# Kernel tuning notes

Hardware: AMD Instinct MI355X
Metric: run time of the kernel (lower is better)

The kernel has to match this reference:

```python
import jax, jax.numpy as jnp
import numpy as np
import math

NUM_HEAD = 16
HEAD_DIM = 64  # hidden_dim 1024 / 16 heads


def setup_inputs() -> dict:
    key = jax.random.key(0)
    ks = jax.random.split(key, 7)
    N, D = 4096, 1024
    s = 1.0 / math.sqrt(D)
    return {
        "node_emb": jax.random.normal(ks[0], (N, D), jnp.float32),
        "Wq": jax.random.normal(ks[1], (D, D), jnp.float32) * s,
        "bq": jax.random.normal(ks[2], (D,), jnp.float32) * 0.01,
        "Wk": jax.random.normal(ks[3], (D, D), jnp.float32) * s,
        "bk": jax.random.normal(ks[4], (D,), jnp.float32) * 0.01,
        "Wv": jax.random.normal(ks[5], (D, D), jnp.float32) * s,
        "bv": jax.random.normal(ks[6], (D,), jnp.float32) * 0.01,
    }


def reference(node_emb, Wq, bq, Wk, bk, Wv, bv):
    N = node_emb.shape[0]
    # QKV projections (Linear: x @ W^T-style; here W stored [in, out])
    q = (node_emb @ Wq + bq).reshape(N, NUM_HEAD, HEAD_DIM)
    k = (node_emb @ Wk + bk).reshape(N, NUM_HEAD, HEAD_DIM)
    v = (node_emb @ Wv + bv).reshape(N, NUM_HEAD, HEAD_DIM)
    # scores: [h, n_query, n_key]
    scale = 1.0 / math.sqrt(HEAD_DIM)
    scores = jnp.einsum("nhd,mhd->hnm", q, k) * scale
    attn = jax.nn.softmax(scores, axis=-1)
    out = jnp.einsum("hnm,mhd->nhd", attn, v)  # [n, h, d]
    return out.reshape(N, NUM_HEAD * HEAD_DIM)
```

## Files before the change

### kernel.cpp

```cpp
#include <hip/hip_runtime.h>
#include <hip/hip_bf16.h>

#define N_NODES 4096
#define DMODEL  1024
#define NHEAD   16
#define HDIM    64
#define NOUT    3072

typedef __attribute__((ext_vector_type(8))) short short8v;
typedef __attribute__((ext_vector_type(4))) float f32x4;
typedef __attribute__((ext_vector_type(16))) float f32x16;
typedef __attribute__((ext_vector_type(4))) unsigned short ushort4v;
typedef __attribute__((ext_vector_type(4))) unsigned int u32x4;

static __device__ __forceinline__ void gload_lds16(const void* g, void* l) {
  __builtin_amdgcn_global_load_lds((const __attribute__((address_space(1))) void*)g,
                                   (__attribute__((address_space(3))) void*)l, 16, 0, 0);
}

static __device__ __forceinline__ unsigned cvtpk(float a, float b) {
  unsigned r;
  asm("v_cvt_pk_bf16_f32 %0, %1, %2" : "=v"(r) : "v"(a), "v"(b));
  return r;
}

__global__ void cvt_x_kernel(const float* __restrict__ x, __hip_bfloat16* __restrict__ xb) {
  int i = blockIdx.x * blockDim.x + threadIdx.x;
  float4 v = ((const float4*)x)[i];
  union { ushort4v u; __hip_bfloat16 h[4]; } o;
  o.h[0] = __float2bfloat16(v.x);
  o.h[1] = __float2bfloat16(v.y);
  o.h[2] = __float2bfloat16(v.z);
  o.h[3] = __float2bfloat16(v.w);
  ((ushort4v*)xb)[i] = o.u;
}

__global__ void transpose_w_kernel(const float* __restrict__ Wq, const float* __restrict__ Wk,
                                   const float* __restrict__ Wv, __hip_bfloat16* __restrict__ WT) {
  __shared__ float tile[32][33];
  const float* W = blockIdx.z == 0 ? Wq : (blockIdx.z == 1 ? Wk : Wv);
  int o0 = blockIdx.x * 32, i0 = blockIdx.y * 32;
  int tx = threadIdx.x, ty = threadIdx.y;
#pragma unroll
  for (int j = 0; j < 32; j += 8)
    tile[ty + j][tx] = W[(size_t)(i0 + ty + j) * DMODEL + o0 + tx];
  __syncthreads();
  __hip_bfloat16* outp = WT + (size_t)blockIdx.z * DMODEL * DMODEL;
#pragma unroll
  for (int j = 0; j < 32; j += 8)
    outp[(size_t)(o0 + ty + j) * DMODEL + i0 + tx] = __float2bfloat16(tile[tx][ty + j]);
}

__global__ __launch_bounds__(256, 2) void gemm_qkv_kernel(
    const __hip_bfloat16* __restrict__ X, const __hip_bfloat16* __restrict__ WT,
    const float* __restrict__ bq, const float* __restrict__ bk, const float* __restrict__ bv,
    __hip_bfloat16* __restrict__ Qo, __hip_bfloat16* __restrict__ Ko, __hip_bfloat16* __restrict__ Vt) {
  __shared__ __hip_bfloat16 As[128 * 32];
  __shared__ __hip_bfloat16 Bs[128 * 32];
  const int t = threadIdx.x;
  const int lane = t & 63;
  const int w = t >> 6, wr = w >> 1, wc = w & 1;
  const int bm = blockIdx.y, bn = blockIdx.x;

  f32x4 acc[4][4] = {};

  const int rowA = t >> 2;
  const int koff = (t & 3) * 8;
  const __hip_bfloat16* Ag0 = X + (size_t)(bm * 128 + rowA) * DMODEL + koff;
  const __hip_bfloat16* Ag1 = X + (size_t)(bm * 128 + 64 + rowA) * DMODEL + koff;
  const __hip_bfloat16* Bg0 = WT + (size_t)(bn * 128 + rowA) * DMODEL + koff;
  const __hip_bfloat16* Bg1 = WT + (size_t)(bn * 128 + 64 + rowA) * DMODEL + koff;
  __hip_bfloat16* Al0 = &As[t * 8];
  __hip_bfloat16* Al1 = &As[(t + 256) * 8];
  __hip_bfloat16* Bl0 = &Bs[t * 8];
  __hip_bfloat16* Bl1 = &Bs[(t + 256) * 8];

  const short* As_s = (const short*)As;
  const short* Bs_s = (const short*)Bs;
  const int fr = lane & 15, fk = (lane >> 4) * 8;

  for (int kt = 0; kt < DMODEL / 32; ++kt) {
    gload_lds16(Ag0 + kt * 32, Al0);
    gload_lds16(Ag1 + kt * 32, Al1);
    gload_lds16(Bg0 + kt * 32, Bl0);
    gload_lds16(Bg1 + kt * 32, Bl1);
    __syncthreads();
    short8v a[4], b[4];
#pragma unroll
    for (int m = 0; m < 4; ++m)
      a[m] = *(const short8v*)&As_s[(wr * 64 + m * 16 + fr) * 32 + fk];
#pragma unroll
    for (int n = 0; n < 4; ++n)
      b[n] = *(const short8v*)&Bs_s[(wc * 64 + n * 16 + fr) * 32 + fk];
#pragma unroll
    for (int m = 0; m < 4; ++m)
#pragma unroll
      for (int n = 0; n < 4; ++n)
        acc[m][n] = __builtin_amdgcn_mfma_f32_16x16x32_bf16(a[m], b[n], acc[m][n], 0, 0, 0);
    __syncthreads();
  }

  const int row0 = bm * 128 + wr * 64;
  const int col0 = bn * 128 + wc * 64;
  const int which = col0 >> 10;
  const float* bias = which == 0 ? bq : (which == 1 ? bk : bv);
  const float QSCALE = 0.18033688011112042f;
#pragma unroll
  for (int m = 0; m < 4; ++m) {
#pragma unroll
    for (int n = 0; n < 4; ++n) {
#pragma unroll
      for (int i = 0; i < 4; ++i) {
        int r = row0 + m * 16 + (lane >> 4) * 4 + i;
        int c = col0 + n * 16 + (lane & 15);
        int oo = c & 1023;
        float v = acc[m][n][i] + bias[oo];
        if (which == 0) v *= QSCALE;
        int h = oo >> 6, d = oo & 63;
        __hip_bfloat16 hv = __float2bfloat16(v);
        if (which == 0)      Qo[((size_t)h << 18) + r * 64 + d] = hv;
        else if (which == 1) Ko[((size_t)h << 18) + r * 64 + d] = hv;
        else                 Vt[((size_t)h << 18) + d * 4096 + r] = hv;
      }
    }
  }
}

__global__ __launch_bounds__(256, 2) void attn64_kernel(
    const __hip_bfloat16* __restrict__ Q, const __hip_bfloat16* __restrict__ K,
    const __hip_bfloat16* __restrict__ Vt,
    __hip_bfloat16* __restrict__ Opart, float* __restrict__ lpart) {
  __shared__ __align__(16) short lds_k[2][64 * 64];
  __shared__ __align__(16) short lds_v[2][64 * 64];

  const int bid = blockIdx.x;
  const int lin = (bid & 7) * 64 + (bid >> 3);
  const int h = lin >> 5, qb = (lin & 31) >> 1, split = lin & 1;

  const int t = threadIdx.x, lane = t & 63, w = t >> 6;
  const int lq = lane & 31, hi = lane >> 5;

  const short* Qh = (const short*)Q + ((size_t)h << 18);
  const short* Kh = (const short*)K + ((size_t)h << 18);
  const short* Vh = (const short*)Vt + ((size_t)h << 18);

  const int q0 = qb * 256 + w * 64;

  short8v qfA[4], qfB[4];
#pragma unroll
  for (int kk = 0; kk < 4; ++kk) {
    qfA[kk] = *(const short8v*)&Qh[(q0 + lq) * 64 + kk * 16 + hi * 8];
    qfB[kk] = *(const short8v*)&Qh[(q0 + 32 + lq) * 64 + kk * 16 + hi * 8];
  }

  int off8[2][4];
#pragma unroll
  for (int half = 0; half < 2; ++half)
#pragma unroll
    for (int kk = 0; kk < 4; ++kk)
      off8[half][kk] = (half * 32 + lq) * 64 + (((kk * 2 + hi) ^ (lq & 7)) * 8);

  auto stage = [&](int kt, int b) {
#pragma unroll
    for (int i = 0; i < 2; ++i) {
      int c = w * 128 + i * 64 + lane;
      int row = c >> 3, ss = (c & 7) ^ (row & 7);
      gload_lds16(Kh + (size_t)(kt * 64 + row) * 64 + ss * 8, &lds_k[b][c * 8]);
    }
#pragma unroll
    for (int i = 0; i < 2; ++i) {
      int c = w * 128 + i * 64 + lane;
      int row = c >> 3, ss = (c & 7) ^ (row & 7);
      gload_lds16(Vh + (size_t)row * 4096 + kt * 64 + ss * 8, &lds_v[b][c * 8]);
    }
  };

  f32x16 oA0 = {}, oA1 = {}, oB0 = {}, oB1 = {};
  float lA_r = 0.f, lB_r = 0.f;

  const int NT = 32;
  const int kt0 = split * NT;

  stage(kt0, 0);

  for (int it = 0; it < NT; ++it) {
    const int cur = it & 1;
    __builtin_amdgcn_s_barrier();
    if (it + 1 < NT) {
      stage(kt0 + it + 1, cur ^ 1);
      asm volatile("s_waitcnt vmcnt(4)" ::: "memory");
    } else {
      asm volatile("s_waitcnt vmcnt(0)" ::: "memory");
    }
    __builtin_amdgcn_s_barrier();
    __builtin_amdgcn_sched_barrier(0);

    const short* kp = lds_k[cur];
    const short* vp = lds_v[cur];

    f32x16 sA0 = {}, sA1 = {}, sB0 = {}, sB1 = {};
    __builtin_amdgcn_s_setprio(1);
#pragma unroll
    for (int kk = 0; kk < 4; ++kk) {
      short8v ka0 = *(const short8v*)&kp[off8[0][kk]];
      sA0 = __builtin_amdgcn_mfma_f32_32x32x16_bf16(ka0, qfA[kk], sA0, 0, 0, 0);
      sB0 = __builtin_amdgcn_mfma_f32_32x32x16_bf16(ka0, qfB[kk], sB0, 0, 0, 0);
      short8v ka1 = *(const short8v*)&kp[off8[1][kk]];
      sA1 = __builtin_amdgcn_mfma_f32_32x32x16_bf16(ka1, qfA[kk], sA1, 0, 0, 0);
      sB1 = __builtin_amdgcn_mfma_f32_32x32x16_bf16(ka1, qfB[kk], sB1, 0, 0, 0);
    }
    __builtin_amdgcn_s_setprio(0);

    short8v paA[4], paB[4];
    {
#pragma unroll
      for (int j = 0; j < 16; ++j) { sA0[j] = __builtin_amdgcn_exp2f(sA0[j]); lA_r += sA0[j]; }
#pragma unroll
      for (int j = 0; j < 16; ++j) { sA1[j] = __builtin_amdgcn_exp2f(sA1[j]); lA_r += sA1[j]; }
#pragma unroll
      for (int half = 0; half < 2; ++half) {
        const f32x16& s = half ? sA1 : sA0;
#pragma unroll
        for (int g = 0; g < 2; ++g) {
          unsigned a0 = cvtpk(s[g * 8 + 0], s[g * 8 + 1]), a1 = cvtpk(s[g * 8 + 2], s[g * 8 + 3]);
          unsigned b0 = cvtpk(s[g * 8 + 4], s[g * 8 + 5]), b1 = cvtpk(s[g * 8 + 6], s[g * 8 + 7]);
          asm volatile("v_permlane32_swap_b32 %0, %1" : "+v"(a0), "+v"(b0));
          asm volatile("v_permlane32_swap_b32 %0, %1" : "+v"(a1), "+v"(b1));
          u32x4 u = {a0, a1, b0, b1};
          paA[half * 2 + g] = __builtin_bit_cast(short8v, u);
        }
      }
#pragma unroll
      for (int j = 0; j < 16; ++j) { sB0[j] = __builtin_amdgcn_exp2f(sB0[j]); lB_r += sB0[j]; }
#pragma unroll
      for (int j = 0; j < 16; ++j) { sB1[j] = __builtin_amdgcn_exp2f(sB1[j]); lB_r += sB1[j]; }
#pragma unroll
      for (int half = 0; half < 2; ++half) {
        const f32x16& s = half ? sB1 : sB0;
#pragma unroll
        for (int g = 0; g < 2; ++g) {
          unsigned a0 = cvtpk(s[g * 8 + 0], s[g * 8 + 1]), a1 = cvtpk(s[g * 8 + 2], s[g * 8 + 3]);
          unsigned b0 = cvtpk(s[g * 8 + 4], s[g * 8 + 5]), b1 = cvtpk(s[g * 8 + 6], s[g * 8 + 7]);
          asm volatile("v_permlane32_swap_b32 %0, %1" : "+v"(a0), "+v"(b0));
          asm volatile("v_permlane32_swap_b32 %0, %1" : "+v"(a1), "+v"(b1));
          u32x4 u = {a0, a1, b0, b1};
          paB[half * 2 + g] = __builtin_bit_cast(short8v, u);
        }
      }
    }

    __builtin_amdgcn_s_setprio(1);
#pragma unroll
    for (int kk = 0; kk < 4; ++kk) {
      short8v vb0 = *(const short8v*)&vp[off8[0][kk]];
      oA0 = __builtin_amdgcn_mfma_f32_32x32x16_bf16(paA[kk], vb0, oA0, 0, 0, 0);
      oB0 = __builtin_amdgcn_mfma_f32_32x32x16_bf16(paB[kk], vb0, oB0, 0, 0, 0);
      short8v vb1 = *(const short8v*)&vp[off8[1][kk]];
      oA1 = __builtin_amdgcn_mfma_f32_32x32x16_bf16(paA[kk], vb1, oA1, 0, 0, 0);
      oB1 = __builtin_amdgcn_mfma_f32_32x32x16_bf16(paB[kk], vb1, oB1, 0, 0, 0);
    }
    __builtin_amdgcn_s_setprio(0);
  }

  {
    float lA = lA_r + __shfl_xor(lA_r, 32);
    float lB = lB_r + __shfl_xor(lB_r, 32);
    if (hi == 0) {
      lpart[((split * NHEAD + h) << 12) + q0 + lq] = lA;
      lpart[((split * NHEAD + h) << 12) + q0 + 32 + lq] = lB;
    }
    __hip_bfloat16* Op = Opart + (size_t)split * N_NODES * DMODEL;
#pragma unroll
    for (int r = 0; r < 16; ++r) {
      int ql = (r & 3) + 8 * (r >> 2) + 4 * hi;
      int qgA = q0 + ql, qgB = q0 + 32 + ql;
      Op[(size_t)qgA * DMODEL + (h << 6) + lq] = __float2bfloat16(oA0[r]);
      Op[(size_t)qgA * DMODEL + (h << 6) + 32 + lq] = __float2bfloat16(oA1[r]);
      Op[(size_t)qgB * DMODEL + (h << 6) + lq] = __float2bfloat16(oB0[r]);
      Op[(size_t)qgB * DMODEL + (h << 6) + 32 + lq] = __float2bfloat16(oB1[r]);
    }
  }
}

__global__ void combine_kernel(const __hip_bfloat16* __restrict__ Opart,
                               const float* __restrict__ lpart,
                               float* __restrict__ out) {
  int idx = blockIdx.x * 256 + threadIdx.x;
  int n = idx >> 8;
  int c4 = idx & 255;
  int h = c4 >> 4;
  float l0 = lpart[(h << 12) + n];
  float l1 = lpart[(NHEAD << 12) + (h << 12) + n];
  float inv = 1.0f / (l0 + l1);
  ushort4v a = ((const ushort4v*)Opart)[idx];
  ushort4v b = ((const ushort4v*)(Opart + (size_t)N_NODES * DMODEL))[idx];
  f32x4 o;
#pragma unroll
  for (int j = 0; j < 4; ++j) {
    float fa = __uint_as_float((unsigned)(unsigned short)a[j] << 16);
    float fb = __uint_as_float((unsigned)(unsigned short)b[j] << 16);
    o[j] = (fa + fb) * inv;
  }
  ((f32x4*)out)[idx] = o;
}

__global__ __launch_bounds__(256, 2) void attn_single_kernel(
    const __hip_bfloat16* __restrict__ Q, const __hip_bfloat16* __restrict__ K,
    const __hip_bfloat16* __restrict__ Vt, float* __restrict__ out) {
  __shared__ __align__(16) short lds_k[2][64 * 64];
  __shared__ __align__(16) short lds_v[2][64 * 64];
  __shared__ float smc[4][32];
  const int bid = blockIdx.x;
  const int lin = (bid & 7) * 64 + (bid >> 3);
  const int h = lin >> 5, qb = lin & 31;
  const int t = threadIdx.x, lane = t & 63, w = t >> 6;
  const int lq = lane & 31, hi = lane >> 5;
  const short* Qh = (const short*)Q + ((size_t)h << 18);
  const short* Kh = (const short*)K + ((size_t)h << 18);
  const short* Vh = (const short*)Vt + ((size_t)h << 18);
  const int q0 = qb * 128 + w * 32;
  short8v qf[4];
#pragma unroll
  for (int kk = 0; kk < 4; ++kk)
    qf[kk] = *(const short8v*)&Qh[(q0 + lq) * 64 + kk * 16 + hi * 8];
  int off8[2][4];
#pragma unroll
  for (int half = 0; half < 2; ++half)
#pragma unroll
    for (int kk = 0; kk < 4; ++kk)
      off8[half][kk] = (half * 32 + lq) * 64 + (((kk * 2 + hi) ^ (lq & 7)) * 8);
  auto stage = [&](int kt, int b) {
#pragma unroll
    for (int i = 0; i < 2; ++i) {
      int c = w * 128 + i * 64 + lane;
      int row = c >> 3, ss = (c & 7) ^ (row & 7);
      gload_lds16(Kh + (size_t)(kt * 64 + row) * 64 + ss * 8, &lds_k[b][c * 8]);
    }
#pragma unroll
    for (int i = 0; i < 2; ++i) {
      int c = w * 128 + i * 64 + lane;
      int row = c >> 3, ss = (c & 7) ^ (row & 7);
      gload_lds16(Vh + (size_t)row * 4096 + kt * 64 + ss * 8, &lds_v[b][c * 8]);
    }
  };
  f32x16 o0 = {}, o1 = {};
  float l_r = 0.f;
  stage(0, 0);
  for (int kt = 0; kt < 64; ++kt) {
    const int cur = kt & 1;
    __builtin_amdgcn_s_barrier();
    if (kt + 1 < 64) {
      stage(kt + 1, cur ^ 1);
      asm volatile("s_waitcnt vmcnt(4)" ::: "memory");
    } else {
      asm volatile("s_waitcnt vmcnt(0)" ::: "memory");
    }
    __builtin_amdgcn_s_barrier();
    __builtin_amdgcn_sched_barrier(0);
    const short* kp = lds_k[cur];
    const short* vp = lds_v[cur];
    f32x16 s0 = {}, s1 = {};
#pragma unroll
    for (int kk = 0; kk < 4; ++kk) {
      short8v ka0 = *(const short8v*)&kp[off8[0][kk]];
      s0 = __builtin_amdgcn_mfma_f32_32x32x16_bf16(ka0, qf[kk], s0, 0, 0, 0);
      short8v ka1 = *(const short8v*)&kp[off8[1][kk]];
      s1 = __builtin_amdgcn_mfma_f32_32x32x16_bf16(ka1, qf[kk], s1, 0, 0, 0);
    }
#pragma unroll
    for (int j = 0; j < 16; ++j) { s0[j] = __builtin_amdgcn_exp2f(s0[j]); l_r += s0[j]; }
#pragma unroll
    for (int j = 0; j < 16; ++j) { s1[j] = __builtin_amdgcn_exp2f(s1[j]); l_r += s1[j]; }
    short8v pa[4];
#pragma unroll
    for (int half = 0; half < 2; ++half) {
      const f32x16& s = half ? s1 : s0;
#pragma unroll
      for (int g = 0; g < 2; ++g) {
        unsigned a0 = cvtpk(s[g * 8 + 0], s[g * 8 + 1]), a1 = cvtpk(s[g * 8 + 2], s[g * 8 + 3]);
        unsigned b0 = cvtpk(s[g * 8 + 4], s[g * 8 + 5]), b1 = cvtpk(s[g * 8 + 6], s[g * 8 + 7]);
        asm volatile("v_permlane32_swap_b32 %0, %1" : "+v"(a0), "+v"(b0));
        asm volatile("v_permlane32_swap_b32 %0, %1" : "+v"(a1), "+v"(b1));
        u32x4 u = {a0, a1, b0, b1};
        pa[half * 2 + g] = __builtin_bit_cast(short8v, u);
      }
    }
#pragma unroll
    for (int kk = 0; kk < 4; ++kk) {
      short8v vb0 = *(const short8v*)&vp[off8[0][kk]];
      o0 = __builtin_amdgcn_mfma_f32_32x32x16_bf16(pa[kk], vb0, o0, 0, 0, 0);
      short8v vb1 = *(const short8v*)&vp[off8[1][kk]];
      o1 = __builtin_amdgcn_mfma_f32_32x32x16_bf16(pa[kk], vb1, o1, 0, 0, 0);
    }
  }
  {
    float lt = l_r + __shfl_xor(l_r, 32);
    float inv = 1.0f / lt;
    if (lane < 32) smc[w][lq] = inv;
#pragma unroll
    for (int r = 0; r < 16; ++r) {
      int ql = (r & 3) + 8 * (r >> 2) + 4 * hi;
      float iv = smc[w][ql];
      int qg = q0 + ql;
      out[(size_t)qg * DMODEL + (h << 6) + lq] = o0[r] * iv;
      out[(size_t)qg * DMODEL + (h << 6) + 32 + lq] = o1[r] * iv;
    }
  }
}

extern "C" void kernel_launch(void* const* d_in, const int* in_sizes, int n_in,
                              void* d_out, int out_size, void* d_ws, size_t ws_size,
                              hipStream_t stream) {
  const float* node_emb = (const float*)d_in[0];
  const float* Wq = (const float*)d_in[1];
  const float* bq = (const float*)d_in[2];
  const float* Wk = (const float*)d_in[3];
  const float* bk = (const float*)d_in[4];
  const float* Wv = (const float*)d_in[5];
  const float* bv = (const float*)d_in[6];
  float* out = (float*)d_out;

  __hip_bfloat16* Xbf = (__hip_bfloat16*)d_ws;
  __hip_bfloat16* WT  = Xbf + (size_t)N_NODES * DMODEL;
  __hip_bfloat16* Qb  = WT + (size_t)NOUT * DMODEL;
  __hip_bfloat16* Kb  = Qb + (size_t)NHEAD * N_NODES * HDIM;
  __hip_bfloat16* Vtb = Kb + (size_t)NHEAD * N_NODES * HDIM;

  const size_t base_bytes =
      ((size_t)N_NODES * DMODEL + (size_t)NOUT * DMODEL +
       3 * (size_t)NHEAD * N_NODES * HDIM) * sizeof(__hip_bfloat16);
  const size_t opart_bytes = 2 * (size_t)N_NODES * DMODEL * sizeof(__hip_bfloat16);
  const size_t lpart_bytes = 2 * (size_t)NHEAD * N_NODES * sizeof(float);
  const bool can_split = ws_size >= base_bytes + opart_bytes + lpart_bytes;

  cvt_x_kernel<<<(N_NODES * DMODEL) / (256 * 4), 256, 0, stream>>>(node_emb, Xbf);
  transpose_w_kernel<<<dim3(32, 32, 3), dim3(32, 8), 0, stream>>>(Wq, Wk, Wv, WT);
  gemm_qkv_kernel<<<dim3(NOUT / 128, N_NODES / 128), 256, 0, stream>>>(
      Xbf, WT, bq, bk, bv, Qb, Kb, Vtb);

  if (can_split) {
    __hip_bfloat16* Opart = (__hip_bfloat16*)((char*)d_ws + base_bytes);
    float* lpart = (float*)(Opart + 2 * (size_t)N_NODES * DMODEL);
    attn64_kernel<<<512, 256, 0, stream>>>(Qb, Kb, Vtb, Opart, lpart);
    combine_kernel<<<(N_NODES * DMODEL) / (256 * 4), 256, 0, stream>>>(Opart, lpart, out);
  } else {
    attn_single_kernel<<<512, 256, 0, stream>>>(Qb, Kb, Vtb, out);
  }
}
```

Measured before the change: 135.0 us.

## Split attention KV range four ways and reuse workspace for partials

Result: slower. 453.0 us (+235.6%).

```diff
diff --git a/kernel.cpp b/kernel.cpp
--- a/kernel.cpp
+++ b/kernel.cpp
@@ -126,7 +126,7 @@
   }
 }
 
-__global__ __launch_bounds__(256, 2) void attn64_kernel(
+__global__ __launch_bounds__(256, 4) void attn64_kernel(
     const __hip_bfloat16* __restrict__ Q, const __hip_bfloat16* __restrict__ K,
     const __hip_bfloat16* __restrict__ Vt,
     __hip_bfloat16* __restrict__ Opart, float* __restrict__ lpart) {
@@ -134,8 +134,8 @@
   __shared__ __align__(16) short lds_v[2][64 * 64];
 
   const int bid = blockIdx.x;
-  const int lin = (bid & 7) * 64 + (bid >> 3);
-  const int h = lin >> 5, qb = (lin & 31) >> 1, split = lin & 1;
+  const int lin = (bid & 7) * 128 + (bid >> 3);
+  const int h = lin >> 6, qb = (lin & 63) >> 2, split = lin & 3;
 
   const int t = threadIdx.x, lane = t & 63, w = t >> 6;
   const int lq = lane & 31, hi = lane >> 5;
@@ -178,7 +178,7 @@
   f32x16 oA0 = {}, oA1 = {}, oB0 = {}, oB1 = {};
   float lA_r = 0.f, lB_r = 0.f;
 
-  const int NT = 32;
+  const int NT = 16;
   const int kt0 = split * NT;
 
   stage(kt0, 0);
@@ -289,19 +289,19 @@
   int n = idx >> 8;
   int c4 = idx & 255;
   int h = c4 >> 4;
-  float l0 = lpart[(h << 12) + n];
-  float l1 = lpart[(NHEAD << 12) + (h << 12) + n];
-  float inv = 1.0f / (l0 + l1);
-  ushort4v a = ((const ushort4v*)Opart)[idx];
-  ushort4v b = ((const ushort4v*)(Opart + (size_t)N_NODES * DMODEL))[idx];
-  f32x4 o;
-#pragma unroll
-  for (int j = 0; j < 4; ++j) {
-    float fa = __uint_as_float((unsigned)(unsigned short)a[j] << 16);
-    float fb = __uint_as_float((unsigned)(unsigned short)b[j] << 16);
-    o[j] = (fa + fb) * inv;
-  }
-  ((f32x4*)out)[idx] = o;
+  float l = 0.f;
+#pragma unroll
+  for (int s = 0; s < 4; ++s) l += lpart[((s * NHEAD + h) << 12) + n];
+  float inv = 1.0f / l;
+  f32x4 o = {};
+#pragma unroll
+  for (int s = 0; s < 4; ++s) {
+    ushort4v a = ((const ushort4v*)(Opart + (size_t)s * N_NODES * DMODEL))[idx];
+#pragma unroll
+    for (int j = 0; j < 4; ++j)
+      o[j] += __uint_as_float((unsigned)(unsigned short)a[j] << 16);
+  }
+  ((f32x4*)out)[idx] = o * inv;
 }
 
 __global__ __launch_bounds__(256, 2) void attn_single_kernel(
@@ -420,18 +420,22 @@
   const float* bv = (const float*)d_in[6];
   float* out = (float*)d_out;
 
-  __hip_bfloat16* Xbf = (__hip_bfloat16*)d_ws;
+  const size_t HSZ = (size_t)NHEAD * N_NODES * HDIM;
+  __hip_bfloat16* Qb  = (__hip_bfloat16*)d_ws;
+  __hip_bfloat16* Kb  = Qb + HSZ;
+  __hip_bfloat16* Vtb = Kb + HSZ;
+  __hip_bfloat16* Xbf = Vtb + HSZ;
   __hip_bfloat16* WT  = Xbf + (size_t)N_NODES * DMODEL;
-  __hip_bfloat16* Qb  = WT + (size_t)NOUT * DMODEL;
-  __hip_bfloat16* Kb  = Qb + (size_t)NHEAD * N_NODES * HDIM;
-  __hip_bfloat16* Vtb = Kb + (size_t)NHEAD * N_NODES * HDIM;
-
+
+  __hip_bfloat16* Opart = Xbf;
+  float* lpart = (float*)(Opart + 4 * (size_t)N_NODES * DMODEL);
+
+  const size_t split_bytes =
+      (3 * HSZ + 4 * (size_t)N_NODES * DMODEL) * sizeof(__hip_bfloat16) +
+      4 * (size_t)NHEAD * N_NODES * sizeof(float);
   const size_t base_bytes =
-      ((size_t)N_NODES * DMODEL + (size_t)NOUT * DMODEL +
-       3 * (size_t)NHEAD * N_NODES * HDIM) * sizeof(__hip_bfloat16);
-  const size_t opart_bytes = 2 * (size_t)N_NODES * DMODEL * sizeof(__hip_bfloat16);
-  const size_t lpart_bytes = 2 * (size_t)NHEAD * N_NODES * sizeof(float);
-  const bool can_split = ws_size >= base_bytes + opart_bytes + lpart_bytes;
+      (3 * HSZ + (size_t)N_NODES * DMODEL + (size_t)NOUT * DMODEL) * sizeof(__hip_bfloat16);
+  const bool can_split = ws_size >= (split_bytes > base_bytes ? split_bytes : base_bytes);
 
   cvt_x_kernel<<<(N_NODES * DMODEL) / (256 * 4), 256, 0, stream>>>(node_emb, Xbf);
   transpose_w_kernel<<<dim3(32, 32, 3), dim3(32, 8), 0, stream>>>(Wq, Wk, Wv, WT);
@@ -439,9 +443,7 @@
       Xbf, WT, bq, bk, bv, Qb, Kb, Vtb);
 
   if (can_split) {
-    __hip_bfloat16* Opart = (__hip_bfloat16*)((char*)d_ws + base_bytes);
-    float* lpart = (float*)(Opart + 2 * (size_t)N_NODES * DMODEL);
-    attn64_kernel<<<512, 256, 0, stream>>>(Qb, Kb, Vtb, Opart, lpart);
+    attn64_kernel<<<1024, 256, 0, stream>>>(Qb, Kb, Vtb, Opart, lpart);
     combine_kernel<<<(N_NODES * DMODEL) / (256 * 4), 256, 0, stream>>>(Opart, lpart, out);
   } else {
     attn_single_kernel<<<512, 256, 0, stream>>>(Qb, Kb, Vtb, out);
```

## Stage two KV tiles per barrier and vectorize weight transpose, alias workspace

Applied to the files above, without the earlier changes.

Result: no change. 134.5 us (-0.4%).

```diff
diff --git a/kernel.cpp b/kernel.cpp
--- a/kernel.cpp
+++ b/kernel.cpp
@@ -41,14 +41,19 @@
   const float* W = blockIdx.z == 0 ? Wq : (blockIdx.z == 1 ? Wk : Wv);
   int o0 = blockIdx.x * 32, i0 = blockIdx.y * 32;
   int tx = threadIdx.x, ty = threadIdx.y;
-#pragma unroll
-  for (int j = 0; j < 32; j += 8)
-    tile[ty + j][tx] = W[(size_t)(i0 + ty + j) * DMODEL + o0 + tx];
+  {
+    float4 v = *(const float4*)&W[(size_t)(i0 + ty) * DMODEL + o0 + tx * 4];
+    tile[ty][tx * 4 + 0] = v.x;
+    tile[ty][tx * 4 + 1] = v.y;
+    tile[ty][tx * 4 + 2] = v.z;
+    tile[ty][tx * 4 + 3] = v.w;
+  }
   __syncthreads();
   __hip_bfloat16* outp = WT + (size_t)blockIdx.z * DMODEL * DMODEL;
-#pragma unroll
-  for (int j = 0; j < 32; j += 8)
-    outp[(size_t)(o0 + ty + j) * DMODEL + i0 + tx] = __float2bfloat16(tile[tx][ty + j]);
+  union { ushort4v u; __hip_bfloat16 h[4]; } o;
+#pragma unroll
+  for (int c = 0; c < 4; ++c) o.h[c] = __float2bfloat16(tile[tx * 4 + c][ty]);
+  *(ushort4v*)&outp[(size_t)(o0 + ty) * DMODEL + i0 + tx * 4] = o.u;
 }
 
 __global__ __launch_bounds__(256, 2) void gemm_qkv_kernel(
@@ -130,8 +135,8 @@
     const __hip_bfloat16* __restrict__ Q, const __hip_bfloat16* __restrict__ K,
     const __hip_bfloat16* __restrict__ Vt,
     __hip_bfloat16* __restrict__ Opart, float* __restrict__ lpart) {
-  __shared__ __align__(16) short lds_k[2][64 * 64];
-  __shared__ __align__(16) short lds_v[2][64 * 64];
+  __shared__ __align__(16) short lds_k[2][2][64 * 64];
+  __shared__ __align__(16) short lds_v[2][2][64 * 64];
 
   const int bid = blockIdx.x;
   const int lin = (bid & 7) * 64 + (bid >> 3);
@@ -160,46 +165,26 @@
     for (int kk = 0; kk < 4; ++kk)
       off8[half][kk] = (half * 32 + lq) * 64 + (((kk * 2 + hi) ^ (lq & 7)) * 8);
 
-  auto stage = [&](int kt, int b) {
+  auto stage = [&](int kt, int p, int s) {
 #pragma unroll
     for (int i = 0; i < 2; ++i) {
       int c = w * 128 + i * 64 + lane;
       int row = c >> 3, ss = (c & 7) ^ (row & 7);
-      gload_lds16(Kh + (size_t)(kt * 64 + row) * 64 + ss * 8, &lds_k[b][c * 8]);
+      gload_lds16(Kh + (size_t)(kt * 64 + row) * 64 + ss * 8, &lds_k[p][s][c * 8]);
     }
 #pragma unroll
     for (int i = 0; i < 2; ++i) {
       int c = w * 128 + i * 64 + lane;
       int row = c >> 3, ss = (c & 7) ^ (row & 7);
-      gload_lds16(Vh + (size_t)row * 4096 + kt * 64 + ss * 8, &lds_v[b][c * 8]);
+      gload_lds16(Vh + (size_t)row * 4096 + kt * 64 + ss * 8, &lds_v[p][s][c * 8]);
     }
   };
 
   f32x16 oA0 = {}, oA1 = {}, oB0 = {}, oB1 = {};
   float lA_r = 0.f, lB_r = 0.f;
 
-  const int NT = 32;
-  const int kt0 = split * NT;
-
-  stage(kt0, 0);
-
-  for (int it = 0; it < NT; ++it) {
-    const int cur = it & 1;
-    __builtin_amdgcn_s_barrier();
-    if (it + 1 < NT) {
-      stage(kt0 + it + 1, cur ^ 1);
-      asm volatile("s_waitcnt vmcnt(4)" ::: "memory");
-    } else {
-      asm volatile("s_waitcnt vmcnt(0)" ::: "memory");
-    }
-    __builtin_amdgcn_s_barrier();
-    __builtin_amdgcn_sched_barrier(0);
-
-    const short* kp = lds_k[cur];
-    const short* vp = lds_v[cur];
-
+  auto compute = [&](const short* kp, const short* vp) {
     f32x16 sA0 = {}, sA1 = {}, sB0 = {}, sB1 = {};
-    __builtin_amdgcn_s_setprio(1);
 #pragma unroll
     for (int kk = 0; kk < 4; ++kk) {
       short8v ka0 = *(const short8v*)&kp[off8[0][kk]];
@@ -209,47 +194,41 @@
       sA1 = __builtin_amdgcn_mfma_f32_32x32x16_bf16(ka1, qfA[kk], sA1, 0, 0, 0);
       sB1 = __builtin_amdgcn_mfma_f32_32x32x16_bf16(ka1, qfB[kk], sB1, 0, 0, 0);
     }
-    __builtin_amdgcn_s_setprio(0);
-
     short8v paA[4], paB[4];
-    {
-#pragma unroll
-      for (int j = 0; j < 16; ++j) { sA0[j] = __builtin_amdgcn_exp2f(sA0[j]); lA_r += sA0[j]; }
-#pragma unroll
-      for (int j = 0; j < 16; ++j) { sA1[j] = __builtin_amdgcn_exp2f(sA1[j]); lA_r += sA1[j]; }
-#pragma unroll
-      for (int half = 0; half < 2; ++half) {
-        const f32x16& s = half ? sA1 : sA0;
-#pragma unroll
-        for (int g = 0; g < 2; ++g) {
-          unsigned a0 = cvtpk(s[g * 8 + 0], s[g * 8 + 1]), a1 = cvtpk(s[g * 8 + 2], s[g * 8 + 3]);
-          unsigned b0 = cvtpk(s[g * 8 + 4], s[g * 8 + 5]), b1 = cvtpk(s[g * 8 + 6], s[g * 8 + 7]);
-          asm volatile("v_permlane32_swap_b32 %0, %1" : "+v"(a0), "+v"(b0));
-          asm volatile("v_permlane32_swap_b32 %0, %1" : "+v"(a1), "+v"(b1));
-          u32x4 u = {a0, a1, b0, b1};
-          paA[half * 2 + g] = __builtin_bit_cast(short8v, u);
-        }
+#pragma unroll
+    for (int j = 0; j < 16; ++j) { sA0[j] = __builtin_amdgcn_exp2f(sA0[j]); lA_r += sA0[j]; }
+#pragma unroll
+    for (int j = 0; j < 16; ++j) { sA1[j] = __builtin_amdgcn_exp2f(sA1[j]); lA_r += sA1[j]; }
+#pragma unroll
+    for (int half = 0; half < 2; ++half) {
+      const f32x16& s = half ? sA1 : sA0;
+#pragma unroll
+      for (int g = 0; g < 2; ++g) {
+        unsigned a0 = cvtpk(s[g * 8 + 0], s[g * 8 + 1]), a1 = cvtpk(s[g * 8 + 2], s[g * 8 + 3]);
+        unsigned b0 = cvtpk(s[g * 8 + 4], s[g * 8 + 5]), b1 = cvtpk(s[g * 8 + 6], s[g * 8 + 7]);
+        asm volatile("v_permlane32_swap_b32 %0, %1" : "+v"(a0), "+v"(b0));
+        asm volatile("v_permlane32_swap_b32 %0, %1" : "+v"(a1), "+v"(b1));
+        u32x4 u = {a0, a1, b0, b1};
+        paA[half * 2 + g] = __builtin_bit_cast(short8v, u);
       }
-#pragma unroll
-      for (int j = 0; j < 16; ++j) { sB0[j] = __builtin_amdgcn_exp2f(sB0[j]); lB_r += sB0[j]; }
-#pragma unroll
-      for (int j = 0; j < 16; ++j) { sB1[j] = __builtin_amdgcn_exp2f(sB1[j]); lB_r += sB1[j]; }
-#pragma unroll
-      for (int half = 0; half < 2; ++half) {
-        const f32x16& s = half ? sB1 : sB0;
-#pragma unroll
-        for (int g = 0; g < 2; ++g) {
-          unsigned a0 = cvtpk(s[g * 8 + 0], s[g * 8 + 1]), a1 = cvtpk(s[g * 8 + 2], s[g * 8 + 3]);
-          unsigned b0 = cvtpk(s[g * 8 + 4], s[g * 8 + 5]), b1 = cvtpk(s[g * 8 + 6], s[g * 8 + 7]);
-          asm volatile("v_permlane32_swap_b32 %0, %1" : "+v"(a0), "+v"(b0));
-          asm volatile("v_permlane32_swap_b32 %0, %1" : "+v"(a1), "+v"(b1));
-          u32x4 u = {a0, a1, b0, b1};
-          paB[half * 2 + g] = __builtin_bit_cast(short8v, u);
-        }
+    }
+#pragma unroll
+    for (int j = 0; j < 16; ++j) { sB0[j] = __builtin_amdgcn_exp2f(sB0[j]); lB_r += sB0[j]; }
+#pragma unroll
+    for (int j = 0; j < 16; ++j) { sB1[j] = __builtin_amdgcn_exp2f(sB1[j]); lB_r += sB1[j]; }
+#pragma unroll
+    for (int half = 0; half < 2; ++half) {
+      const f32x16& s = half ? sB1 : sB0;
+#pragma unroll
+      for (int g = 0; g < 2; ++g) {
+        unsigned a0 = cvtpk(s[g * 8 + 0], s[g * 8 + 1]), a1 = cvtpk(s[g * 8 + 2], s[g * 8 + 3]);
+        unsigned b0 = cvtpk(s[g * 8 + 4], s[g * 8 + 5]), b1 = cvtpk(s[g * 8 + 6], s[g * 8 + 7]);
+        asm volatile("v_permlane32_swap_b32 %0, %1" : "+v"(a0), "+v"(b0));
+        asm volatile("v_permlane32_swap_b32 %0, %1" : "+v"(a1), "+v"(b1));
+        u32x4 u = {a0, a1, b0, b1};
+        paB[half * 2 + g] = __builtin_bit_cast(short8v, u);
       }
     }
-
-    __builtin_amdgcn_s_setprio(1);
 #pragma unroll
     for (int kk = 0; kk < 4; ++kk) {
       short8v vb0 = *(const short8v*)&vp[off8[0][kk]];
@@ -259,7 +238,29 @@
       oA1 = __builtin_amdgcn_mfma_f32_32x32x16_bf16(paA[kk], vb1, oA1, 0, 0, 0);
       oB1 = __builtin_amdgcn_mfma_f32_32x32x16_bf16(paB[kk], vb1, oB1, 0, 0, 0);
     }
-    __builtin_amdgcn_s_setprio(0);
+  };
+
+  const int NT = 32;
+  const int NIV = NT / 2;
+  const int kt0 = split * NT;
+
+  stage(kt0 + 0, 0, 0);
+  stage(kt0 + 1, 0, 1);
+
+  for (int iv = 0; iv < NIV; ++iv) {
+    const int p = iv & 1;
+    __builtin_amdgcn_s_barrier();
+    if (iv + 1 < NIV) {
+      stage(kt0 + 2 * iv + 2, p ^ 1, 0);
+      stage(kt0 + 2 * iv + 3, p ^ 1, 1);
+      asm volatile("s_waitcnt vmcnt(8)" ::: "memory");
+    } else {
+      asm volatile("s_waitcnt vmcnt(0)" ::: "memory");
+    }
+    __builtin_amdgcn_s_barrier();
+    __builtin_amdgcn_sched_barrier(0);
+    compute(lds_k[p][0], lds_v[p][0]);
+    compute(lds_k[p][1], lds_v[p][1]);
   }
 
   {
@@ -420,27 +421,29 @@
   const float* bv = (const float*)d_in[6];
   float* out = (float*)d_out;
 
-  __hip_bfloat16* Xbf = (__hip_bfloat16*)d_ws;
+  const size_t HSZ = (size_t)NHEAD * N_NODES * HDIM;
+  __hip_bfloat16* Qb  = (__hip_bfloat16*)d_ws;
+  __hip_bfloat16* Kb  = Qb + HSZ;
+  __hip_bfloat16* Vtb = Kb + HSZ;
+  __hip_bfloat16* Xbf = Vtb + HSZ;
   __hip_bfloat16* WT  = Xbf + (size_t)N_NODES * DMODEL;
-  __hip_bfloat16* Qb  = WT + (size_t)NOUT * DMODEL;
-  __hip_bfloat16* Kb  = Qb + (size_t)NHEAD * N_NODES * HDIM;
-  __hip_bfloat16* Vtb = Kb + (size_t)NHEAD * N_NODES * HDIM;
-
+
+  __hip_bfloat16* Opart = Xbf;
+  float* lpart = (float*)(Opart + 2 * (size_t)N_NODES * DMODEL);
+
+  const size_t split_bytes =
+      (3 * HSZ + 2 * (size_t)N_NODES * DMODEL) * sizeof(__hip_bfloat16) +
+      2 * (size_t)NHEAD * N_NODES * sizeof(float);
   const size_t base_bytes =
-      ((size_t)N_NODES * DMODEL + (size_t)NOUT * DMODEL +
-       3 * (size_t)NHEAD * N_NODES * HDIM) * sizeof(__hip_bfloat16);
-  const size_t opart_bytes = 2 * (size_t)N_NODES * DMODEL * sizeof(__hip_bfloat16);
-  const size_t lpart_bytes = 2 * (size_t)NHEAD * N_NODES * sizeof(float);
-  const bool can_split = ws_size >= base_bytes + opart_bytes + lpart_bytes;
+      (3 * HSZ + (size_t)N_NODES * DMODEL + (size_t)NOUT * DMODEL) * sizeof(__hip_bfloat16);
+  const bool can_split = ws_size >= (split_bytes > base_bytes ? split_bytes : base_bytes);
 
   cvt_x_kernel<<<(N_NODES * DMODEL) / (256 * 4), 256, 0, stream>>>(node_emb, Xbf);
-  transpose_w_kernel<<<dim3(32, 32, 3), dim3(32, 8), 0, stream>>>(Wq, Wk, Wv, WT);
+  transpose_w_kernel<<<dim3(32, 32, 3), dim3(8, 32), 0, stream>>>(Wq, Wk, Wv, WT);
   gemm_qkv_kernel<<<dim3(NOUT / 128, N_NODES / 128), 256, 0, stream>>>(
       Xbf, WT, bq, bk, bv, Qb, Kb, Vtb);
 
   if (can_split) {
-    __hip_bfloat16* Opart = (__hip_bfloat16*)((char*)d_ws + base_bytes);
-    float* lpart = (float*)(Opart + 2 * (size_t)N_NODES * DMODEL);
     attn64_kernel<<<512, 256, 0, stream>>>(Qb, Kb, Vtb, Opart, lpart);
     combine_kernel<<<(N_NODES * DMODEL) / (256 * 4), 256, 0, stream>>>(Opart, lpart, out);
   } else {
```
